# Optimization experiments

Measured on AMD Instinct MI355X. Metric: run time of the kernel, lower is better.

## Reference

```python
import jax, jax.numpy as jnp
import numpy as np

NF = 32      # feature channels
DG = 4       # deformable groups
K = 9        # 3x3 kernel taps


def _conv(x, w, b, stride=1):
    # x: [B,C,H,W], w: [O,I,3,3] (pad=1)
    y = jax.lax.conv_general_dilated(x, w, (stride, stride), ((1, 1), (1, 1)),
                                     dimension_numbers=('NCHW', 'OIHW', 'NCHW'))
    return y + b[None, :, None, None]


def _lrelu(x):
    return jnp.where(x >= 0, x, 0.1 * x)


def _up2(x):
    # bilinear, align_corners=False (half-pixel centers, matches torch F.interpolate)
    B, C, H, W = x.shape
    return jax.image.resize(x, (B, C, 2 * H, 2 * W), method='bilinear')


def _deform_conv(x, om, w, b):
    # Modulated deformable conv (DCNv2), stride=1, pad=1, dilation=1, 3x3.
    # x: [B,C,H,W]; om: [B,3*DG*K,H,W] = (offset_y | offset_x | mask) blocks.
    B, C, H, W = x.shape
    Cg = C // DG
    o1, o2, m = jnp.split(om, 3, axis=1)
    off_y = o1.reshape(B, DG, K, H, W)
    off_x = o2.reshape(B, DG, K, H, W)
    mask = jax.nn.sigmoid(m).reshape(B, DG, K, H, W)
    k = jnp.arange(K)
    dy = (k // 3 - 1).astype(x.dtype)            # kernel tap y displacement
    dx = (k % 3 - 1).astype(x.dtype)
    # sampling positions [B,DG,K,H,W]
    py = off_y + jnp.arange(H, dtype=x.dtype)[:, None] + dy[:, None, None]
    px = off_x + jnp.arange(W, dtype=x.dtype)[None, :] + dx[:, None, None]
    y0 = jnp.floor(py)
    x0 = jnp.floor(px)
    wy1 = py - y0
    wx1 = px - x0
    y0i = y0.astype(jnp.int32)
    x0i = x0.astype(jnp.int32)
    imgf = x.reshape(B, DG, Cg, H * W)

    def corner(yi, xi, wt):
        valid = (yi >= 0) & (yi < H) & (xi >= 0) & (xi < W)
        yc = jnp.clip(yi, 0, H - 1)
        xc = jnp.clip(xi, 0, W - 1)
        idx = (yc * W + xc).reshape(B, DG, 1, K * H * W)
        v = jnp.take_along_axis(imgf, idx, axis=3).reshape(B, DG, Cg, K, H, W)
        return v * (wt * valid)[:, :, None]

    samp = (corner(y0i, x0i, (1 - wy1) * (1 - wx1))
            + corner(y0i, x0i + 1, (1 - wy1) * wx1)
            + corner(y0i + 1, x0i, wy1 * (1 - wx1))
            + corner(y0i + 1, x0i + 1, wy1 * wx1))
    samp = samp * mask[:, :, None]                       # [B,DG,Cg,K,H,W]
    out = jnp.einsum('bgckhw,ogck->bohw', samp, w.reshape(w.shape[0], DG, Cg, K))
    return out + b[None, :, None, None]


_PARAM_SHAPES = [
    ('w1_1', (32, 64, 3, 3)), ('b1_1', (32,)),
    ('w2_1', (32, 32, 3, 3)), ('b2_1', (32,)),
    ('w3_1', (32, 32, 3, 3)), ('b3_1', (32,)),
    ('w4_1', (32, 32, 3, 3)), ('b4_1', (32,)),
    ('w6_1', (32, 32, 3, 3)), ('b6_1', (32,)),
    ('w7_1', (32, 32, 3, 3)), ('b7_1', (32,)),
    ('w1_2', (32, 64, 3, 3)), ('b1_2', (32,)),
    ('w2_2', (32, 32, 3, 3)), ('b2_2', (32,)),
    ('w3_2', (32, 64, 3, 3)), ('b3_2', (32,)),
    ('w4_2', (32, 32, 3, 3)), ('b4_2', (32,)),
    ('w_om', (108, 32, 3, 3)), ('b_om', (108,)),   # DCN_sep conv_offset_mask: 3*DG*K=108
    ('w_dcn', (32, 32, 3, 3)), ('b_dcn', (32,)),
]


def setup_inputs() -> dict:
    key = jax.random.key(0)
    ks = jax.random.split(key, len(_PARAM_SHAPES) + 2)
    B, H, W = 4, 192, 192
    d = {
        'fea1': jax.random.normal(ks[0], (B, NF, H, W), jnp.float32),
        'fea2': jax.random.normal(ks[1], (B, NF, H, W), jnp.float32),
    }
    for i, (name, shp) in enumerate(_PARAM_SHAPES):
        d[name] = jax.random.normal(ks[i + 2], shp, jnp.float32) * 0.05
    return d


def reference(fea1, fea2, w1_1, b1_1, w2_1, b2_1, w3_1, b3_1, w4_1, b4_1,
              w6_1, b6_1, w7_1, b7_1, w1_2, b1_2, w2_2, b2_2, w3_2, b3_2,
              w4_2, b4_2, w_om, b_om, w_dcn, b_dcn):
    off = _lrelu(_conv(jnp.concatenate([fea1, fea2], 1), w1_1, b1_1))
    off1 = _lrelu(_conv(off, w2_1, b2_1))
    off2 = _lrelu(_conv(off1, w3_1, b3_1, 2))   # H/2
    off2 = _lrelu(_conv(off2, w4_1, b4_1))
    off3 = _lrelu(_conv(off2, w6_1, b6_1, 2))   # H/4
    off3 = _lrelu(_conv(off3, w7_1, b7_1))
    up = _up2(off3)                              # back to H/2
    off = _lrelu(_conv(jnp.concatenate([up, off2], 1), w1_2, b1_2))
    off = _lrelu(_conv(off, w2_2, b2_2))
    up = _up2(off)                               # back to H
    off = _lrelu(_conv(jnp.concatenate([up, off1], 1), w3_2, b3_2))
    base_offset = _conv(off, w4_2, b4_2)
    om = _conv(base_offset, w_om, b_om)          # DCN_sep offset/mask head
    return _deform_conv(fea2, om, w_dcn, b_dcn)
```

## Files before the change

### kernel.cpp

```cpp
#include <hip/hip_runtime.h>
#include <math.h>


#define BDIM 256

typedef __attribute__((ext_vector_type(8))) short short8v;
typedef __attribute__((ext_vector_type(4))) float f32x4;

__device__ __forceinline__ unsigned short f2bf(float f) {
    unsigned u = __builtin_bit_cast(unsigned, f);
    u = (u + 0x7FFF + ((u >> 16) & 1)) >> 16;
    return (unsigned short)u;
}
__device__ __forceinline__ float bf2f(unsigned short h) {
    unsigned u = ((unsigned)h) << 16;
    return __builtin_bit_cast(float, u);
}

template<int NPASS, int NHALF, int NT, int STRIDE, bool LRELU>
__global__ __launch_bounds__(BDIM, 4)
void convm_k(const short* __restrict__ in0, const short* __restrict__ in1,
             const short* __restrict__ wf,
             const float* __restrict__ bias,
             short* __restrict__ out,
             int Hin, int Win, int Hout, int Wout, int OCS, int coutTot,
             int nhTot)
{
    const int lane = threadIdx.x & 63;
    const int wid  = blockIdx.x * 4 + (threadIdx.x >> 6);
    const int segs = Wout / (16 * NT);
    const int b  = wid / (Hout * segs);
    int r = wid - b * (Hout * segs);
    const int oy = r / segs;
    const int x0 = (r - oy * segs) * (16 * NT);
    const int lp = lane & 15;
    const int g  = lane >> 4;
    const int hBase = blockIdx.z * NHALF;
    const int coutBase = blockIdx.z * NHALF * 16;

    int rowOff[3]; bool rowOk[3];
#pragma unroll
    for (int ty = 0; ty < 3; ++ty) {
        const int iy = oy * STRIDE + ty - 1;
        rowOk[ty] = (unsigned)iy < (unsigned)Hin;
        rowOff[ty] = min(max(iy, 0), Hin - 1) * Win;
    }
    int colOff[3][NT]; bool colOk[3][NT];
#pragma unroll
    for (int tx = 0; tx < 3; ++tx)
#pragma unroll
        for (int nt = 0; nt < NT; ++nt) {
            const int ix = (x0 + nt * 16 + lp) * STRIDE + tx - 1;
            colOk[tx][nt] = (unsigned)ix < (unsigned)Win;
            colOff[tx][nt] = min(max(ix, 0), Win - 1) * 32 + g * 8;
        }

    f32x4 acc[NT][NHALF];
#pragma unroll
    for (int nt = 0; nt < NT; ++nt)
#pragma unroll
        for (int h = 0; h < NHALF; ++h)
            acc[nt][h] = (f32x4){0.f, 0.f, 0.f, 0.f};

    const size_t inPlane = (size_t)Hin * Win * 32;
    const short8v zero = {};

#pragma unroll
    for (int pass = 0; pass < NPASS; ++pass) {
        const short* inp = (pass == 0 ? in0 : in1) + (size_t)b * inPlane;

        short8v bcur[NT];
#pragma unroll
        for (int nt = 0; nt < NT; ++nt) {
            short8v v = *(const short8v*)(inp + (size_t)rowOff[0] * 32 + colOff[0][nt]);
            bcur[nt] = (rowOk[0] & colOk[0][nt]) ? v : zero;
        }

#pragma unroll
        for (int t = 0; t < 9; ++t) {
            short8v bnxt[NT];
            if (t < 8) {
                const int ty = (t + 1) / 3, tx = (t + 1) % 3;
#pragma unroll
                for (int nt = 0; nt < NT; ++nt) {
                    short8v v = *(const short8v*)(inp + (size_t)rowOff[ty] * 32 + colOff[tx][nt]);
                    bnxt[nt] = (rowOk[ty] & colOk[tx][nt]) ? v : zero;
                }
            }
#pragma unroll
            for (int h = 0; h < NHALF; ++h) {
                short8v av = *(const short8v*)(
                    wf + ((((size_t)pass * 9 + t) * nhTot + hBase + h) * 64 + lane) * 8);
#pragma unroll
                for (int nt = 0; nt < NT; ++nt)
                    acc[nt][h] = __builtin_amdgcn_mfma_f32_16x16x32_bf16(
                        av, bcur[nt], acc[nt][h], 0, 0, 0);
            }
            if (t < 8) {
#pragma unroll
                for (int nt = 0; nt < NT; ++nt) bcur[nt] = bnxt[nt];
            }
        }
    }

    const size_t outBase = ((size_t)b * Hout + oy) * Wout;
#pragma unroll
    for (int nt = 0; nt < NT; ++nt) {
        const int p = x0 + nt * 16 + lp;
        short* op = out + (outBase + p) * OCS;
#pragma unroll
        for (int h = 0; h < NHALF; ++h) {
            const int co0 = coutBase + h * 16 + g * 4;
            ushort4 st;
#pragma unroll
            for (int j = 0; j < 4; ++j) {
                float v = acc[nt][h][j] + bias[min(co0 + j, coutTot - 1)];
                if (LRELU) v = (v >= 0.f) ? v : 0.1f * v;
                ((unsigned short*)&st)[j] = f2bf(v);
            }
            if (co0 < coutTot)
                *(ushort4*)(op + co0) = st;
        }
    }
}

struct WPArgs {
    const float* src[11];
    int off[11];
    int npass[11], nhalf[11], O[11];
};

__global__ __launch_bounds__(BDIM)
void wprep_k(WPArgs a, short* __restrict__ wbase)
{
    const int z = blockIdx.z;
    const int n = a.npass[z] * 9 * a.nhalf[z] * 512;
    const int idx = blockIdx.x * BDIM + threadIdx.x;
    if (idx >= n) return;
    const int j = idx & 7;
    const int l = (idx >> 3) & 63;
    int r = idx >> 9;
    const int h = r % a.nhalf[z]; r /= a.nhalf[z];
    const int t = r % 9;
    const int pass = r / 9;
    const int I = a.npass[z] * 32;
    const int cout = h * 16 + (l & 15);
    const int cin  = pass * 32 + (l >> 4) * 8 + j;
    float v = (cout < a.O[z]) ? a.src[z][((size_t)cout * I + cin) * 9 + t] : 0.f;
    wbase[a.off[z] + idx] = (short)f2bf(v);
}

__global__ __launch_bounds__(BDIM)
void wdp_k(const float* __restrict__ w, short* __restrict__ dst)
{
    const int idx = blockIdx.x * BDIM + threadIdx.x;
    if (idx >= 9 * 2 * 64 * 8) return;
    const int j = idx & 7;
    const int l = (idx >> 3) & 63;
    const int h = (idx >> 9) & 1;
    const int k = idx >> 10;
    const int cout = h * 16 + (l & 15);
    const int cin  = (l >> 4) * 8 + j;
    dst[idx] = (short)f2bf(w[((size_t)cout * 32 + cin) * 9 + k]);
}

__global__ __launch_bounds__(BDIM)
void cvtnhwc_k(const float* __restrict__ s0, const float* __restrict__ s1,
               short* __restrict__ d0, short* __restrict__ d1, int H, int W)
{
    const float* s = blockIdx.z ? s1 : s0;
    short* d = blockIdx.z ? d1 : d0;
    const int idx = blockIdx.x * BDIM + threadIdx.x;
    if (idx >= 4 * 32 * H * W) return;
    const int c = idx & 31;
    int t = idx >> 5;
    const int x = t % W; t /= W;
    const int y = t % H;
    const int b = t / H;
    d[idx] = (short)f2bf(s[(((size_t)b * 32 + c) * H + y) * W + x]);
}

__global__ __launch_bounds__(BDIM)
void up2b_k(const short* __restrict__ in, short* __restrict__ out,
            int Hin, int Win)
{
    const int Hout = 2 * Hin, Wout = 2 * Win;
    const int idx = blockIdx.x * BDIM + threadIdx.x;
    if (idx >= 4 * Hout * Wout * 4) return;
    const int cg = idx & 3;
    int t = idx >> 2;
    const int x = t % Wout; t /= Wout;
    const int y = t % Hout;
    const int b = t / Hout;

    const float sy = (y + 0.5f) * 0.5f - 0.5f;
    const float sx = (x + 0.5f) * 0.5f - 0.5f;
    const float y0f = floorf(sy), x0f = floorf(sx);
    const float wy = sy - y0f, wx = sx - x0f;
    const int y0 = (int)y0f, x0 = (int)x0f;
    const int y0c = min(max(y0, 0), Hin - 1);
    const int y1c = min(max(y0 + 1, 0), Hin - 1);
    const int x0c = min(max(x0, 0), Win - 1);
    const int x1c = min(max(x0 + 1, 0), Win - 1);

    const short* base = in + (size_t)b * Hin * Win * 32 + cg * 8;
    short8v v00 = *(const short8v*)(base + ((size_t)y0c * Win + x0c) * 32);
    short8v v01 = *(const short8v*)(base + ((size_t)y0c * Win + x1c) * 32);
    short8v v10 = *(const short8v*)(base + ((size_t)y1c * Win + x0c) * 32);
    short8v v11 = *(const short8v*)(base + ((size_t)y1c * Win + x1c) * 32);

    short8v o;
#pragma unroll
    for (int j = 0; j < 8; ++j) {
        float f = (1.f - wy) * ((1.f - wx) * bf2f((unsigned short)v00[j]) +
                                wx * bf2f((unsigned short)v01[j]))
                + wy * ((1.f - wx) * bf2f((unsigned short)v10[j]) +
                        wx * bf2f((unsigned short)v11[j]));
        o[j] = (short)f2bf(f);
    }
    short* op = out + (size_t)b * Hout * Wout * 32 + ((size_t)y * Wout + x) * 32 + cg * 8;
    *(short8v*)op = o;
}

__global__ __launch_bounds__(BDIM, 4)
void dcnm_k(const short* __restrict__ xb,
            const short* __restrict__ om,
            const short* __restrict__ wf,
            const float* __restrict__ bias,
            float* __restrict__ out, int H, int W)
{
    const int lane = threadIdx.x & 63;
    const int wid  = blockIdx.x * 4 + (threadIdx.x >> 6);
    const int segs = W / 16;
    const int b = wid / (H * segs);
    int r = wid - b * (H * segs);
    const int y = r / segs;
    const int x = (r - y * segs) * 16 + (lane & 15);
    const int g = lane >> 4;
    const size_t plane = (size_t)H * W;

    f32x4 acc0 = (f32x4){0.f, 0.f, 0.f, 0.f};
    f32x4 acc1 = (f32x4){0.f, 0.f, 0.f, 0.f};

    const short* omb = om + ((size_t)b * plane + (size_t)y * W + x) * 112;
    const short* xbb = xb + (size_t)b * plane * 32 + g * 8;

#pragma unroll
    for (int k = 0; k < 9; ++k) {
        const float offy = bf2f((unsigned short)omb[g * 9 + k]);
        const float offx = bf2f((unsigned short)omb[36 + g * 9 + k]);
        const float ml   = bf2f((unsigned short)omb[72 + g * 9 + k]);
        const float m = 1.f / (1.f + __expf(-ml));

        const float py = offy + (float)y + (float)(k / 3 - 1);
        const float px = offx + (float)x + (float)(k % 3 - 1);
        const float y0f = floorf(py), x0f = floorf(px);
        const int y0 = (int)y0f, x0 = (int)x0f;
        const float wy1 = py - y0f, wx1 = px - x0f;
        const float wy0 = 1.f - wy1, wx0 = 1.f - wx1;

        const bool y0ok = (unsigned)y0 < (unsigned)H;
        const bool y1ok = (unsigned)(y0 + 1) < (unsigned)H;
        const bool x0ok = (unsigned)x0 < (unsigned)W;
        const bool x1ok = (unsigned)(x0 + 1) < (unsigned)W;
        const int y0c = min(max(y0, 0), H - 1);
        const int y1c = min(max(y0 + 1, 0), H - 1);
        const int x0c = min(max(x0, 0), W - 1);
        const int x1c = min(max(x0 + 1, 0), W - 1);

        const float w00 = wy0 * wx0 * ((y0ok && x0ok) ? 1.f : 0.f) * m;
        const float w01 = wy0 * wx1 * ((y0ok && x1ok) ? 1.f : 0.f) * m;
        const float w10 = wy1 * wx0 * ((y1ok && x0ok) ? 1.f : 0.f) * m;
        const float w11 = wy1 * wx1 * ((y1ok && x1ok) ? 1.f : 0.f) * m;

        short8v v00 = *(const short8v*)(xbb + ((size_t)y0c * W + x0c) * 32);
        short8v v01 = *(const short8v*)(xbb + ((size_t)y0c * W + x1c) * 32);
        short8v v10 = *(const short8v*)(xbb + ((size_t)y1c * W + x0c) * 32);
        short8v v11 = *(const short8v*)(xbb + ((size_t)y1c * W + x1c) * 32);

        short8v bv;
#pragma unroll
        for (int j = 0; j < 8; ++j) {
            float s = w00 * bf2f((unsigned short)v00[j])
                    + w01 * bf2f((unsigned short)v01[j])
                    + w10 * bf2f((unsigned short)v10[j])
                    + w11 * bf2f((unsigned short)v11[j]);
            bv[j] = (short)f2bf(s);
        }

        short8v a0 = *(const short8v*)(wf + (((size_t)k * 2 + 0) * 64 + lane) * 8);
        short8v a1 = *(const short8v*)(wf + (((size_t)k * 2 + 1) * 64 + lane) * 8);
        acc0 = __builtin_amdgcn_mfma_f32_16x16x32_bf16(a0, bv, acc0, 0, 0, 0);
        acc1 = __builtin_amdgcn_mfma_f32_16x16x32_bf16(a1, bv, acc1, 0, 0, 0);
    }

    float* op = out + (size_t)b * 32 * plane + (size_t)y * W + x;
#pragma unroll
    for (int j = 0; j < 4; ++j) {
        const int co0 = g * 4 + j;
        const int co1 = 16 + g * 4 + j;
        op[(size_t)co0 * plane] = acc0[j] + bias[co0];
        op[(size_t)co1 * plane] = acc1[j] + bias[co1];
    }
}


extern "C" void kernel_launch(void* const* d_in, const int* in_sizes, int n_in,
                              void* d_out, int out_size, void* d_ws, size_t ws_size,
                              hipStream_t stream)
{
    const float* fea1  = (const float*)d_in[0];
    const float* fea2  = (const float*)d_in[1];
    const float* w1_1  = (const float*)d_in[2];  const float* b1_1 = (const float*)d_in[3];
    const float* w2_1  = (const float*)d_in[4];  const float* b2_1 = (const float*)d_in[5];
    const float* w3_1  = (const float*)d_in[6];  const float* b3_1 = (const float*)d_in[7];
    const float* w4_1  = (const float*)d_in[8];  const float* b4_1 = (const float*)d_in[9];
    const float* w6_1  = (const float*)d_in[10]; const float* b6_1 = (const float*)d_in[11];
    const float* w7_1  = (const float*)d_in[12]; const float* b7_1 = (const float*)d_in[13];
    const float* w1_2  = (const float*)d_in[14]; const float* b1_2 = (const float*)d_in[15];
    const float* w2_2  = (const float*)d_in[16]; const float* b2_2 = (const float*)d_in[17];
    const float* w3_2  = (const float*)d_in[18]; const float* b3_2 = (const float*)d_in[19];
    const float* w4_2  = (const float*)d_in[20]; const float* b4_2 = (const float*)d_in[21];
    const float* w_om  = (const float*)d_in[22]; const float* b_om = (const float*)d_in[23];
    const float* w_dcn = (const float*)d_in[24]; const float* b_dcn= (const float*)d_in[25];

    const int H = 192, W = 192;
    char* ws = (char*)d_ws;

    short* fea1b = (short*)(ws + 0);
    short* fea2b = (short*)(ws + 9437184);
    short* bufA  = (short*)(ws + 18874368);
    short* bufB  = (short*)(ws + 28311552);
    short* bufC  = (short*)(ws + 0);
    short* bufD  = (short*)(ws + 2359296);
    short* bufE  = (short*)(ws + 4718592);
    short* bufF  = (short*)(ws + 5308416);
    short* bufG  = (short*)(ws + 5898240);
    short* bufH  = (short*)(ws + 0);
    short* bufI  = (short*)(ws + 4718592);
    short* bufJ  = (short*)(ws + 37748736);
    short* bufK  = (short*)(ws + 18874368);
    short* bufL  = (short*)(ws + 0);
    short* om    = (short*)(ws + 37748736);
    short* wfrag = (short*)(ws + 70778880);
    short* wfdcn = (short*)(ws + 71092224);

    const int WOFF[11] = {0, 18432, 27648, 36864, 46080, 55296,
                          64512, 82944, 92160, 110592, 119808};

    dim3 blk(BDIM, 1, 1);

    {
        WPArgs a;
        const float* srcs[11] = {w1_1, w2_1, w3_1, w4_1, w6_1, w7_1,
                                 w1_2, w2_2, w3_2, w4_2, w_om};
        const int NP[11] = {2,1,1,1,1,1,2,1,2,1,1};
        const int NH[11] = {2,2,2,2,2,2,2,2,2,2,8};
        const int Os[11] = {32,32,32,32,32,32,32,32,32,32,108};
        for (int i = 0; i < 11; ++i) {
            a.src[i] = srcs[i]; a.off[i] = WOFF[i];
            a.npass[i] = NP[i]; a.nhalf[i] = NH[i]; a.O[i] = Os[i];
        }
        wprep_k<<<dim3(144, 1, 11), blk, 0, stream>>>(a, wfrag);
        cvtnhwc_k<<<dim3(18432, 1, 2), blk, 0, stream>>>(fea1, fea2, fea1b, fea2b, H, W);
        wdp_k<<<dim3(36), blk, 0, stream>>>(w_dcn, wfdcn);
    }

    convm_k<2,2,2,1,true><<<dim3(1152), blk, 0, stream>>>(
        fea1b, fea2b, wfrag + WOFF[0], b1_1, bufA, 192,192,192,192, 32, 32, 2);
    convm_k<1,2,2,1,true><<<dim3(1152), blk, 0, stream>>>(
        bufA, nullptr, wfrag + WOFF[1], b2_1, bufB, 192,192,192,192, 32, 32, 2);
    convm_k<1,2,1,2,true><<<dim3(576), blk, 0, stream>>>(
        bufB, nullptr, wfrag + WOFF[2], b3_1, bufC, 192,192,96,96, 32, 32, 2);
    convm_k<1,2,1,1,true><<<dim3(576), blk, 0, stream>>>(
        bufC, nullptr, wfrag + WOFF[3], b4_1, bufD, 96,96,96,96, 32, 32, 2);
    convm_k<1,2,1,2,true><<<dim3(144), blk, 0, stream>>>(
        bufD, nullptr, wfrag + WOFF[4], b6_1, bufE, 96,96,48,48, 32, 32, 2);
    convm_k<1,2,1,1,true><<<dim3(144), blk, 0, stream>>>(
        bufE, nullptr, wfrag + WOFF[5], b7_1, bufF, 48,48,48,48, 32, 32, 2);
    up2b_k<<<dim3(576), blk, 0, stream>>>(bufF, bufG, 48, 48);
    convm_k<2,2,1,1,true><<<dim3(576), blk, 0, stream>>>(
        bufG, bufD, wfrag + WOFF[6], b1_2, bufH, 96,96,96,96, 32, 32, 2);
    convm_k<1,2,1,1,true><<<dim3(576), blk, 0, stream>>>(
        bufH, nullptr, wfrag + WOFF[7], b2_2, bufI, 96,96,96,96, 32, 32, 2);
    up2b_k<<<dim3(2304), blk, 0, stream>>>(bufI, bufJ, 96, 96);
    convm_k<2,2,2,1,true><<<dim3(1152), blk, 0, stream>>>(
        bufJ, bufB, wfrag + WOFF[8], b3_2, bufK, 192,192,192,192, 32, 32, 2);
    convm_k<1,2,2,1,false><<<dim3(1152), blk, 0, stream>>>(
        bufK, nullptr, wfrag + WOFF[9], b4_2, bufL, 192,192,192,192, 32, 32, 2);
    convm_k<1,2,2,1,false><<<dim3(1152, 1, 4), blk, 0, stream>>>(
        bufL, nullptr, wfrag + WOFF[10], b_om, om, 192,192,192,192, 112, 108, 8);
    dcnm_k<<<dim3(2304), blk, 0, stream>>>(
        fea2b, om, wfdcn, b_dcn, (float*)d_out, H, W);
}
```

Baseline: 337.8 us.

## Fuse offset/mask conv into deformable conv kernel and drop NT tiling

The final 108-channel offset/mask convolution is computed inside the deformable-conv kernel with MFMA, staged through LDS, so the om tensor is never written to or read from global memory. Output-channel padding is reduced from 8 to 7 half-tiles, which shrinks both the weight prep and the MFMA count. The generic conv kernel loses its NT=2 column tiling: each wave now handles 16 pixels, grids double for the full-resolution layers, and all 9 tap loads are issued before the MFMAs instead of being double-buffered. This adds register pressure (9 short8 plus 7 accumulators) and a block barrier to the DCN kernel, and gives up the weight reuse across two pixel tiles.

```diff
diff --git a/kernel.cpp b/kernel.cpp
--- a/kernel.cpp
+++ b/kernel.cpp
@@ -17,26 +17,23 @@
     return __builtin_bit_cast(float, u);
 }
 
-template<int NPASS, int NHALF, int NT, int STRIDE, bool LRELU>
+template<int NPASS, int NHALF, int STRIDE, bool LRELU>
 __global__ __launch_bounds__(BDIM, 4)
 void convm_k(const short* __restrict__ in0, const short* __restrict__ in1,
              const short* __restrict__ wf,
              const float* __restrict__ bias,
              short* __restrict__ out,
-             int Hin, int Win, int Hout, int Wout, int OCS, int coutTot,
-             int nhTot)
+             int Hin, int Win, int Hout, int Wout, int OCS)
 {
     const int lane = threadIdx.x & 63;
     const int wid  = blockIdx.x * 4 + (threadIdx.x >> 6);
-    const int segs = Wout / (16 * NT);
+    const int segs = Wout >> 4;
     const int b  = wid / (Hout * segs);
     int r = wid - b * (Hout * segs);
     const int oy = r / segs;
-    const int x0 = (r - oy * segs) * (16 * NT);
+    const int x0 = (r - oy * segs) * 16;
     const int lp = lane & 15;
     const int g  = lane >> 4;
-    const int hBase = blockIdx.z * NHALF;
-    const int coutBase = blockIdx.z * NHALF * 16;
 
     int rowOff[3]; bool rowOk[3];
 #pragma unroll
@@ -45,22 +42,17 @@
         rowOk[ty] = (unsigned)iy < (unsigned)Hin;
         rowOff[ty] = min(max(iy, 0), Hin - 1) * Win;
     }
-    int colOff[3][NT]; bool colOk[3][NT];
-#pragma unroll
-    for (int tx = 0; tx < 3; ++tx)
-#pragma unroll
-        for (int nt = 0; nt < NT; ++nt) {
-            const int ix = (x0 + nt * 16 + lp) * STRIDE + tx - 1;
-            colOk[tx][nt] = (unsigned)ix < (unsigned)Win;
-            colOff[tx][nt] = min(max(ix, 0), Win - 1) * 32 + g * 8;
-        }
-
-    f32x4 acc[NT][NHALF];
-#pragma unroll
-    for (int nt = 0; nt < NT; ++nt)
-#pragma unroll
-        for (int h = 0; h < NHALF; ++h)
-            acc[nt][h] = (f32x4){0.f, 0.f, 0.f, 0.f};
+    int colOff[3]; bool colOk[3];
+#pragma unroll
+    for (int tx = 0; tx < 3; ++tx) {
+        const int ix = (x0 + lp) * STRIDE + tx - 1;
+        colOk[tx] = (unsigned)ix < (unsigned)Win;
+        colOff[tx] = min(max(ix, 0), Win - 1) * 32 + g * 8;
+    }
+
+    f32x4 acc[NHALF];
+#pragma unroll
+    for (int h = 0; h < NHALF; ++h) acc[h] = (f32x4){0.f, 0.f, 0.f, 0.f};
 
     const size_t inPlane = (size_t)Hin * Win * 32;
     const short8v zero = {};
@@ -69,58 +61,36 @@
     for (int pass = 0; pass < NPASS; ++pass) {
         const short* inp = (pass == 0 ? in0 : in1) + (size_t)b * inPlane;
 
-        short8v bcur[NT];
-#pragma unroll
-        for (int nt = 0; nt < NT; ++nt) {
-            short8v v = *(const short8v*)(inp + (size_t)rowOff[0] * 32 + colOff[0][nt]);
-            bcur[nt] = (rowOk[0] & colOk[0][nt]) ? v : zero;
-        }
-
+        short8v bv[9];
 #pragma unroll
         for (int t = 0; t < 9; ++t) {
-            short8v bnxt[NT];
-            if (t < 8) {
-                const int ty = (t + 1) / 3, tx = (t + 1) % 3;
-#pragma unroll
-                for (int nt = 0; nt < NT; ++nt) {
-                    short8v v = *(const short8v*)(inp + (size_t)rowOff[ty] * 32 + colOff[tx][nt]);
-                    bnxt[nt] = (rowOk[ty] & colOk[tx][nt]) ? v : zero;
-                }
-            }
+            const int ty = t / 3, tx = t % 3;
+            short8v v = *(const short8v*)(inp + (size_t)rowOff[ty] * 32 + colOff[tx]);
+            bv[t] = (rowOk[ty] & colOk[tx]) ? v : zero;
+        }
+#pragma unroll
+        for (int t = 0; t < 9; ++t) {
 #pragma unroll
             for (int h = 0; h < NHALF; ++h) {
                 short8v av = *(const short8v*)(
-                    wf + ((((size_t)pass * 9 + t) * nhTot + hBase + h) * 64 + lane) * 8);
-#pragma unroll
-                for (int nt = 0; nt < NT; ++nt)
-                    acc[nt][h] = __builtin_amdgcn_mfma_f32_16x16x32_bf16(
-                        av, bcur[nt], acc[nt][h], 0, 0, 0);
+                    wf + ((((size_t)pass * 9 + t) * NHALF + h) * 64 + lane) * 8);
+                acc[h] = __builtin_amdgcn_mfma_f32_16x16x32_bf16(av, bv[t], acc[h], 0, 0, 0);
             }
-            if (t < 8) {
-#pragma unroll
-                for (int nt = 0; nt < NT; ++nt) bcur[nt] = bnxt[nt];
-            }
-        }
-    }
-
-    const size_t outBase = ((size_t)b * Hout + oy) * Wout;
-#pragma unroll
-    for (int nt = 0; nt < NT; ++nt) {
-        const int p = x0 + nt * 16 + lp;
-        short* op = out + (outBase + p) * OCS;
-#pragma unroll
-        for (int h = 0; h < NHALF; ++h) {
-            const int co0 = coutBase + h * 16 + g * 4;
-            ushort4 st;
-#pragma unroll
-            for (int j = 0; j < 4; ++j) {
-                float v = acc[nt][h][j] + bias[min(co0 + j, coutTot - 1)];
-                if (LRELU) v = (v >= 0.f) ? v : 0.1f * v;
-                ((unsigned short*)&st)[j] = f2bf(v);
-            }
-            if (co0 < coutTot)
-                *(ushort4*)(op + co0) = st;
-        }
+        }
+    }
+
+    short* op = out + (((size_t)b * Hout + oy) * Wout + x0 + lp) * OCS;
+#pragma unroll
+    for (int h = 0; h < NHALF; ++h) {
+        const int co0 = h * 16 + g * 4;
+        ushort4 st;
+#pragma unroll
+        for (int j = 0; j < 4; ++j) {
+            float v = acc[h][j] + bias[co0 + j];
+            if (LRELU) v = (v >= 0.f) ? v : 0.1f * v;
+            ((unsigned short*)&st)[j] = f2bf(v);
+        }
+        *(ushort4*)(op + co0) = st;
     }
 }
 
@@ -224,49 +194,101 @@
 
 __global__ __launch_bounds__(BDIM, 4)
 void dcnm_k(const short* __restrict__ xb,
-            const short* __restrict__ om,
-            const short* __restrict__ wf,
+            const short* __restrict__ bo,
+            const short* __restrict__ wfo,
+            const float* __restrict__ obias,
+            const short* __restrict__ wfd,
             const float* __restrict__ bias,
             float* __restrict__ out, int H, int W)
 {
+    __shared__ unsigned short omld[4][16][112];
+
     const int lane = threadIdx.x & 63;
-    const int wid  = blockIdx.x * 4 + (threadIdx.x >> 6);
-    const int segs = W / 16;
+    const int wv   = threadIdx.x >> 6;
+    const int wid  = blockIdx.x * 4 + wv;
+    const int segs = W >> 4;
     const int b = wid / (H * segs);
     int r = wid - b * (H * segs);
     const int y = r / segs;
-    const int x = (r - y * segs) * 16 + (lane & 15);
-    const int g = lane >> 4;
+    const int x0 = (r - y * segs) * 16;
+    const int lp = lane & 15;
+    const int g  = lane >> 4;
+    const int x  = x0 + lp;
     const size_t plane = (size_t)H * W;
-
-    f32x4 acc0 = (f32x4){0.f, 0.f, 0.f, 0.f};
-    f32x4 acc1 = (f32x4){0.f, 0.f, 0.f, 0.f};
-
-    const short* omb = om + ((size_t)b * plane + (size_t)y * W + x) * 112;
+    const short8v zero = {};
+
+    {
+        int rowOff[3]; bool rowOk[3];
+#pragma unroll
+        for (int ty = 0; ty < 3; ++ty) {
+            const int iy = y + ty - 1;
+            rowOk[ty] = (unsigned)iy < (unsigned)H;
+            rowOff[ty] = min(max(iy, 0), H - 1) * W;
+        }
+        int colOff[3]; bool colOk[3];
+#pragma unroll
+        for (int tx = 0; tx < 3; ++tx) {
+            const int ix = x + tx - 1;
+            colOk[tx] = (unsigned)ix < (unsigned)W;
+            colOff[tx] = min(max(ix, 0), W - 1) * 32 + g * 8;
+        }
+        const short* inp = bo + (size_t)b * plane * 32;
+        short8v bv[9];
+#pragma unroll
+        for (int t = 0; t < 9; ++t) {
+            const int ty = t / 3, tx = t % 3;
+            short8v v = *(const short8v*)(inp + (size_t)rowOff[ty] * 32 + colOff[tx]);
+            bv[t] = (rowOk[ty] & colOk[tx]) ? v : zero;
+        }
+        f32x4 acc[7];
+#pragma unroll
+        for (int h = 0; h < 7; ++h) acc[h] = (f32x4){0.f, 0.f, 0.f, 0.f};
+#pragma unroll
+        for (int t = 0; t < 9; ++t) {
+#pragma unroll
+            for (int h = 0; h < 7; ++h) {
+                short8v av = *(const short8v*)(wfo + (((size_t)t * 7 + h) * 64 + lane) * 8);
+                acc[h] = __builtin_amdgcn_mfma_f32_16x16x32_bf16(av, bv[t], acc[h], 0, 0, 0);
+            }
+        }
+#pragma unroll
+        for (int h = 0; h < 7; ++h) {
+            const int co0 = h * 16 + g * 4;
+            ushort4 st;
+#pragma unroll
+            for (int j = 0; j < 4; ++j)
+                ((unsigned short*)&st)[j] = f2bf(acc[h][j] + obias[min(co0 + j, 107)]);
+            *(ushort4*)&omld[wv][lp][co0] = st;
+        }
+    }
+    __syncthreads();
+
+    f32x4 p0 = (f32x4){0.f, 0.f, 0.f, 0.f};
+    f32x4 p1 = (f32x4){0.f, 0.f, 0.f, 0.f};
     const short* xbb = xb + (size_t)b * plane * 32 + g * 8;
 
 #pragma unroll
     for (int k = 0; k < 9; ++k) {
-        const float offy = bf2f((unsigned short)omb[g * 9 + k]);
-        const float offx = bf2f((unsigned short)omb[36 + g * 9 + k]);
-        const float ml   = bf2f((unsigned short)omb[72 + g * 9 + k]);
+        const float offy = bf2f(omld[wv][lp][g * 9 + k]);
+        const float offx = bf2f(omld[wv][lp][36 + g * 9 + k]);
+        const float ml   = bf2f(omld[wv][lp][72 + g * 9 + k]);
         const float m = 1.f / (1.f + __expf(-ml));
 
         const float py = offy + (float)y + (float)(k / 3 - 1);
         const float px = offx + (float)x + (float)(k % 3 - 1);
         const float y0f = floorf(py), x0f = floorf(px);
-        const int y0 = (int)y0f, x0 = (int)x0f;
+        const int y0 = (int)y0f, x0i = (int)x0f;
         const float wy1 = py - y0f, wx1 = px - x0f;
         const float wy0 = 1.f - wy1, wx0 = 1.f - wx1;
 
         const bool y0ok = (unsigned)y0 < (unsigned)H;
         const bool y1ok = (unsigned)(y0 + 1) < (unsigned)H;
-        const bool x0ok = (unsigned)x0 < (unsigned)W;
-        const bool x1ok = (unsigned)(x0 + 1) < (unsigned)W;
+        const bool x0ok = (unsigned)x0i < (unsigned)W;
+        const bool x1ok = (unsigned)(x0i + 1) < (unsigned)W;
         const int y0c = min(max(y0, 0), H - 1);
         const int y1c = min(max(y0 + 1, 0), H - 1);
-        const int x0c = min(max(x0, 0), W - 1);
-        const int x1c = min(max(x0 + 1, 0), W - 1);
+        const int x0c = min(max(x0i, 0), W - 1);
+        const int x1c = min(max(x0i + 1, 0), W - 1);
 
         const float w00 = wy0 * wx0 * ((y0ok && x0ok) ? 1.f : 0.f) * m;
         const float w01 = wy0 * wx1 * ((y0ok && x1ok) ? 1.f : 0.f) * m;
@@ -288,10 +310,10 @@
             bv[j] = (short)f2bf(s);
         }
 
-        short8v a0 = *(const short8v*)(wf + (((size_t)k * 2 + 0) * 64 + lane) * 8);
-        short8v a1 = *(const short8v*)(wf + (((size_t)k * 2 + 1) * 64 + lane) * 8);
-        acc0 = __builtin_amdgcn_mfma_f32_16x16x32_bf16(a0, bv, acc0, 0, 0, 0);
-        acc1 = __builtin_amdgcn_mfma_f32_16x16x32_bf16(a1, bv, acc1, 0, 0, 0);
+        short8v a0 = *(const short8v*)(wfd + (((size_t)k * 2 + 0) * 64 + lane) * 8);
+        short8v a1 = *(const short8v*)(wfd + (((size_t)k * 2 + 1) * 64 + lane) * 8);
+        p0 = __builtin_amdgcn_mfma_f32_16x16x32_bf16(a0, bv, p0, 0, 0, 0);
+        p1 = __builtin_amdgcn_mfma_f32_16x16x32_bf16(a1, bv, p1, 0, 0, 0);
     }
 
     float* op = out + (size_t)b * 32 * plane + (size_t)y * W + x;
@@ -299,8 +321,8 @@
     for (int j = 0; j < 4; ++j) {
         const int co0 = g * 4 + j;
         const int co1 = 16 + g * 4 + j;
-        op[(size_t)co0 * plane] = acc0[j] + bias[co0];
-        op[(size_t)co1 * plane] = acc1[j] + bias[co1];
+        op[(size_t)co0 * plane] = p0[j] + bias[co0];
+        op[(size_t)co1 * plane] = p1[j] + bias[co1];
     }
 }
 
@@ -341,9 +363,8 @@
     short* bufJ  = (short*)(ws + 37748736);
     short* bufK  = (short*)(ws + 18874368);
     short* bufL  = (short*)(ws + 0);
-    short* om    = (short*)(ws + 37748736);
     short* wfrag = (short*)(ws + 70778880);
-    short* wfdcn = (short*)(ws + 71092224);
+    short* wfdcn = (short*)(ws + 71083008);
 
     const int WOFF[11] = {0, 18432, 27648, 36864, 46080, 55296,
                           64512, 82944, 92160, 110592, 119808};
@@ -355,41 +376,39 @@
         const float* srcs[11] = {w1_1, w2_1, w3_1, w4_1, w6_1, w7_1,
                                  w1_2, w2_2, w3_2, w4_2, w_om};
         const int NP[11] = {2,1,1,1,1,1,2,1,2,1,1};
-        const int NH[11] = {2,2,2,2,2,2,2,2,2,2,8};
+        const int NH[11] = {2,2,2,2,2,2,2,2,2,2,7};
         const int Os[11] = {32,32,32,32,32,32,32,32,32,32,108};
         for (int i = 0; i < 11; ++i) {
             a.src[i] = srcs[i]; a.off[i] = WOFF[i];
             a.npass[i] = NP[i]; a.nhalf[i] = NH[i]; a.O[i] = Os[i];
         }
-        wprep_k<<<dim3(144, 1, 11), blk, 0, stream>>>(a, wfrag);
+        wprep_k<<<dim3(126, 1, 11), blk, 0, stream>>>(a, wfrag);
         cvtnhwc_k<<<dim3(18432, 1, 2), blk, 0, stream>>>(fea1, fea2, fea1b, fea2b, H, W);
         wdp_k<<<dim3(36), blk, 0, stream>>>(w_dcn, wfdcn);
     }
 
-    convm_k<2,2,2,1,true><<<dim3(1152), blk, 0, stream>>>(
-        fea1b, fea2b, wfrag + WOFF[0], b1_1, bufA, 192,192,192,192, 32, 32, 2);
-    convm_k<1,2,2,1,true><<<dim3(1152), blk, 0, stream>>>(
-        bufA, nullptr, wfrag + WOFF[1], b2_1, bufB, 192,192,192,192, 32, 32, 2);
-    convm_k<1,2,1,2,true><<<dim3(576), blk, 0, stream>>>(
-        bufB, nullptr, wfrag + WOFF[2], b3_1, bufC, 192,192,96,96, 32, 32, 2);
-    convm_k<1,2,1,1,true><<<dim3(576), blk, 0, stream>>>(
-        bufC, nullptr, wfrag + WOFF[3], b4_1, bufD, 96,96,96,96, 32, 32, 2);
-    convm_k<1,2,1,2,true><<<dim3(144), blk, 0, stream>>>(
-        bufD, nullptr, wfrag + WOFF[4], b6_1, bufE, 96,96,48,48, 32, 32, 2);
-    convm_k<1,2,1,1,true><<<dim3(144), blk, 0, stream>>>(
-        bufE, nullptr, wfrag + WOFF[5], b7_1, bufF, 48,48,48,48, 32, 32, 2);
+    convm_k<2,2,1,true><<<dim3(2304), blk, 0, stream>>>(
+        fea1b, fea2b, wfrag + WOFF[0], b1_1, bufA, 192,192,192,192, 32);
+    convm_k<1,2,1,true><<<dim3(2304), blk, 0, stream>>>(
+        bufA, nullptr, wfrag + WOFF[1], b2_1, bufB, 192,192,192,192, 32);
+    convm_k<1,2,2,true><<<dim3(576), blk, 0, stream>>>(
+        bufB, nullptr, wfrag + WOFF[2], b3_1, bufC, 192,192,96,96, 32);
+    convm_k<1,2,1,true><<<dim3(576), blk, 0, stream>>>(
+        bufC, nullptr, wfrag + WOFF[3], b4_1, bufD, 96,96,96,96, 32);
+    convm_k<1,2,2,true><<<dim3(144), blk, 0, stream>>>(
+        bufD, nullptr, wfrag + WOFF[4], b6_1, bufE, 96,96,48,48, 32);
+    convm_k<1,2,1,true><<<dim3(144), blk, 0, stream>>>(
+        bufE, nullptr, wfrag + WOFF[5], b7_1, bufF, 48,48,48,48, 32);
     up2b_k<<<dim3(576), blk, 0, stream>>>(bufF, bufG, 48, 48);
-    convm_k<2,2,1,1,true><<<dim3(576), blk, 0, stream>>>(
-        bufG, bufD, wfrag + WOFF[6], b1_2, bufH, 96,96,96,96, 32, 32, 2);
-    convm_k<1,2,1,1,true><<<dim3(576), blk, 0, stream>>>(
-        bufH, nullptr, wfrag + WOFF[7], b2_2, bufI, 96,96,96,96, 32, 32, 2);
+    convm_k<2,2,1,true><<<dim3(576), blk, 0, stream>>>(
+        bufG, bufD, wfrag + WOFF[6], b1_2, bufH, 96,96,96,96, 32);
+    convm_k<1,2,1,true><<<dim3(576), blk, 0, stream>>>(
+        bufH, nullptr, wfrag + WOFF[7], b2_2, bufI, 96,96,96,96, 32);
     up2b_k<<<dim3(2304), blk, 0, stream>>>(bufI, bufJ, 96, 96);
-    convm_k<2,2,2,1,true><<<dim3(1152), blk, 0, stream>>>(
-        bufJ, bufB, wfrag + WOFF[8], b3_2, bufK, 192,192,192,192, 32, 32, 2);
-    convm_k<1,2,2,1,false><<<dim3(1152), blk, 0, stream>>>(
-        bufK, nullptr, wfrag + WOFF[9], b4_2, bufL, 192,192,192,192, 32, 32, 2);
-    convm_k<1,2,2,1,false><<<dim3(1152, 1, 4), blk, 0, stream>>>(
-        bufL, nullptr, wfrag + WOFF[10], b_om, om, 192,192,192,192, 112, 108, 8);
+    convm_k<2,2,1,true><<<dim3(2304), blk, 0, stream>>>(
+        bufJ, bufB, wfrag + WOFF[8], b3_2, bufK, 192,192,192,192, 32);
+    convm_k<1,2,1,false><<<dim3(2304), blk, 0, stream>>>(
+        bufK, nullptr, wfrag + WOFF[9], b4_2, bufL, 192,192,192,192, 32);
     dcnm_k<<<dim3(2304), blk, 0, stream>>>(
-        fea2b, om, wfdcn, b_dcn, (float*)d_out, H, W);
-}
+        fea2b, bufL, wfrag + WOFF[10], b_om, wfdcn, b_dcn, (float*)d_out, H, W);
+}
```

Result: faster. 325.1 us (-3.7%).
